# Performance work log

Measured on AMD Instinct MI355X. Metric: run time of the kernel, lower is better.

Reference implementation:

```python
import jax, jax.numpy as jnp
import numpy as np

RADIUS = 0.4
SIGMA = 0.08
EPS = 1e-5  # InstanceNorm2d default eps
KERNEL_CONDENSE_RATIO = 0.7


def setup_inputs() -> dict:
    key = jax.random.key(0)
    k1, k2, k3, k4, k5 = jax.random.split(key, 5)
    m, b, nc, ks, na, co = 1024, 2, 512, 24, 60, 128
    frag = jax.random.uniform(k1, (m, 3), dtype=jnp.float32)          # fragment points in unit cube
    clouds = jax.random.uniform(k2, (b, 3, nc), dtype=jnp.float32)    # centers (already n_center -> no FPS)
    # kernel points inside ball of KERNEL_CONDENSE_RATIO * radius
    kp = (jax.random.uniform(k3, (ks, 3), dtype=jnp.float32) - 0.5) * 2.0 * (KERNEL_CONDENSE_RATIO * RADIUS)
    # kanchor=60 rotation anchors (random orthonormal frames via QR)
    anchors, _ = jnp.linalg.qr(jax.random.normal(k4, (na, 3, 3), dtype=jnp.float32))
    # rotate kernel points per anchor: (ks, na, 3), matching np.transpose(anchors @ kernels.T, (2,0,1))
    kernels = jnp.einsum('aij,kj->kai', anchors, kp)
    # BasicSO3Conv weight: dim_in=1 -> W [dim_out, ks]
    W = jax.random.normal(k5, (co, ks), dtype=jnp.float32) * (1.0 / np.sqrt(ks))
    return {"frag": frag, "clouds": clouds, "kernels": kernels, "W": W, "anchors": anchors}


def _propagate(frag, clouds, kernels, W):
    # frag [m,3], clouds [b,3,nc], kernels [ks,na,3], W [co,ks]
    c = jnp.transpose(clouds, (0, 2, 1))                 # [b,nc,3]
    diff = frag[None, None] - c[:, :, None]              # [b,nc,m,3] (frag point minus center)
    d2 = jnp.sum(diff * diff, axis=-1)                   # [b,nc,m]
    mask = (d2 < RADIUS * RADIUS).astype(diff.dtype)     # ball query mask
    nnctn = jnp.sum(mask, axis=-1)                       # [b,nc] neighbor counts
    base = jnp.exp(-d2 / SIGMA) * mask                   # shared Gaussian factor, masked [b,nc,m]
    k2 = jnp.sum(kernels * kernels, axis=-1)             # [ks,na]
    na = kernels.shape[1]

    def step(carry, a_idx):
        kpa = kernels[:, a_idx]                          # [ks,3] kernel points for this anchor
        dot = jnp.einsum('bnmd,kd->bnmk', diff, kpa)     # [b,nc,m,ks]
        # exp(-||diff - kp||^2 / sigma) = base * exp((2*dot - |kp|^2)/sigma)
        w = base[..., None] * jnp.exp((2.0 * dot - k2[:, a_idx]) / SIGMA)
        return carry, jnp.sum(w, axis=2)                 # [b,nc,ks]

    _, wts = jax.lax.scan(step, 0, jnp.arange(na))       # [na,b,nc,ks]
    wts = jnp.transpose(wts, (1, 3, 2, 0))               # [b,ks,nc,na]
    wts = wts / (nnctn[:, None, :, None] + 1.0)          # count normalization

    feats = jnp.einsum('ck,bkna->bcna', W, wts)          # BasicSO3Conv (dim_in=1): [b,co,nc,na]
    # InstanceNorm2d(affine=False): per (b, channel) stats over spatial (nc, na)
    mu = jnp.mean(feats, axis=(2, 3), keepdims=True)
    var = jnp.var(feats, axis=(2, 3), keepdims=True)
    feat = (feats - mu) * jax.lax.rsqrt(var + EPS)
    return jax.nn.relu(feat)


def reference(frag, clouds, kernels, W, anchors):
    feat = _propagate(frag, clouds, kernels, W)
    # SphericalPointCloud(xyz=centers, feats, anchors)
    return clouds, feat, anchors
```

## Files before the change

kernel.cpp:

```cpp
#include <hip/hip_runtime.h>
#include <math.h>

#define NC 512
#define NB 2
#define M 1024
#define KS 24
#define NA 60
#define CO 128
#define CELLS 1440
#define CHA 20
#define CCELLS 480
#define NTOT 30720.0f
#define LSCALE 18.033688011112043f
#define R2 0.16f
#define NSLOT 32

#define FEAT_OFF 3072
#define ANCH_OFF (3072 + 7864320)

__device__ __forceinline__ float dot4acc(float s, float4 w, float4 v) {
    return fmaf(w.x, v.x, fmaf(w.y, v.y, fmaf(w.z, v.z, fmaf(w.w, v.w, s))));
}

__launch_bounds__(256)
__global__ void k_wts(const float* __restrict__ frag, const float* __restrict__ clouds,
                      const float* __restrict__ kernels, const float* __restrict__ W,
                      float* __restrict__ wts, float* __restrict__ accum) {
    int bx = blockIdx.x;
    int chunk = bx % 3;
    int bn = bx / 3;
    int b = bn >> 9, n = bn & (NC - 1);
    int tid = threadIdx.x, wave = tid >> 6, lane = tid & 63;
    __shared__ float4 spl[M];
    __shared__ int wcnt[16];
    __shared__ __align__(16) float swl[512];

    int lc0 = tid, lc1 = tid + 256;
    float4 kc0, kc1;
    {
        int cells[2] = {chunk * CCELLS + lc0, chunk * CCELLS + lc1};
        bool vld[2] = {true, lc1 < CCELLS};
        float4* kcs[2] = {&kc0, &kc1};
        #pragma unroll
        for (int q = 0; q < 2; ++q) {
            if (vld[q]) {
                int cell = cells[q];
                int a = cell / KS, k = cell - a * KS;
                const float* kp = kernels + (size_t)(k * NA + a) * 3;
                float kx = kp[0], ky = kp[1], kz = kp[2];
                float k2 = kx * kx + ky * ky + kz * kz;
                *kcs[q] = make_float4(kx * (2.0f * LSCALE), ky * (2.0f * LSCALE),
                                      kz * (2.0f * LSCALE), -k2 * LSCALE);
            } else {
                *kcs[q] = make_float4(0.f, 0.f, 0.f, -1e30f);
            }
        }
    }

    float cx = clouds[b * 3 * NC + n];
    float cy = clouds[b * 3 * NC + NC + n];
    float cz = clouds[b * 3 * NC + 2 * NC + n];

    float dx[4], dy[4], dz[4], ei[4];
    int pos[4];
    bool pr[4];
    unsigned long long lmask = (1ull << lane) - 1ull;
    #pragma unroll
    for (int j = 0; j < 4; ++j) {
        int m = tid + j * 256;
        dx[j] = frag[3 * m]     - cx;
        dy[j] = frag[3 * m + 1] - cy;
        dz[j] = frag[3 * m + 2] - cz;
        float s = __fmul_rn(dx[j], dx[j]);
        s = __fadd_rn(s, __fmul_rn(dy[j], dy[j]));
        s = __fadd_rn(s, __fmul_rn(dz[j], dz[j]));
        pr[j] = s < R2;
        ei[j] = __builtin_amdgcn_exp2f(-s * LSCALE);
        unsigned long long mk = __ballot(pr[j]);
        pos[j] = __popcll(mk & lmask);
        if (lane == 0) wcnt[j * 4 + wave] = __popcll(mk);
    }
    __syncthreads();
    int run = 0, base[4];
    #pragma unroll
    for (int t2 = 0; t2 < 16; ++t2) {
        if ((t2 & 3) == wave) base[t2 >> 2] = run;
        run += wcnt[t2];
    }
    int cnt = run;
    #pragma unroll
    for (int j = 0; j < 4; ++j)
        if (pr[j]) spl[base[j] + pos[j]] = make_float4(dx[j], dy[j], dz[j], ei[j]);
    __syncthreads();

    float acc0 = 0.f, acc1 = 0.f;
    #pragma unroll 2
    for (int i = 0; i < cnt; ++i) {
        float4 p = spl[i];
        float a0 = fmaf(p.x, kc0.x, fmaf(p.y, kc0.y, fmaf(p.z, kc0.z, kc0.w)));
        float a1 = fmaf(p.x, kc1.x, fmaf(p.y, kc1.y, fmaf(p.z, kc1.z, kc1.w)));
        acc0 = fmaf(__builtin_amdgcn_exp2f(a0), p.w, acc0);
        acc1 = fmaf(__builtin_amdgcn_exp2f(a1), p.w, acc1);
    }

    float inv = 1.0f / (float)(cnt + 1);
    float w0 = acc0 * inv, w1 = acc1 * inv;
    float* wrow = wts + (size_t)bn * CELLS + chunk * CCELLS;
    wrow[lc0] = w0;
    swl[lc0] = w0;
    if (lc1 < CCELLS) { wrow[lc1] = w1; swl[lc1] = w1; }
    __syncthreads();

    int c = tid >> 1, ah = tid & 1;
    float4 wr[6];
    {
        const float4* W4 = (const float4*)(W + c * KS);
        #pragma unroll
        for (int j = 0; j < 6; ++j) wr[j] = W4[j];
    }
    float fs = 0.f, fs2 = 0.f;
    #pragma unroll
    for (int i = 0; i < 10; ++i) {
        const float4* v4 = (const float4*)(swl + (ah * 10 + i) * KS);
        float f = 0.f;
        #pragma unroll
        for (int j = 0; j < 6; ++j) f = dot4acc(f, wr[j], v4[j]);
        fs += f;
        fs2 = fmaf(f, f, fs2);
    }
    fs  += __shfl_xor(fs, 1);
    fs2 += __shfl_xor(fs2, 1);
    if (ah == 0) {
        int slot = bx & (NSLOT - 1);
        float* ap = accum + (((size_t)(b * NSLOT + slot) * CO + c) * 2);
        atomicAdd(&ap[0], fs);
        atomicAdd(&ap[1], fs2);
    }
}

__launch_bounds__(256)
__global__ void k_out(const float* __restrict__ wts, const float* __restrict__ W,
                      const float* __restrict__ accum, const float* __restrict__ clouds,
                      const float* __restrict__ anchors, float* __restrict__ out) {
    int bn = blockIdx.x, b = bn >> 9, n = bn & (NC - 1);
    int tid = threadIdx.x, wave = tid >> 6, lane = tid & 63;
    __shared__ __align__(16) float wl[CELLS];
    __shared__ float fl[CO * NA];
    __shared__ float2 sst[CO];

    if (bn < 12) {
        int i = bn * 256 + tid;
        out[i] = clouds[i];
    } else if (bn < 15) {
        int i = (bn - 12) * 256 + tid;
        if (i < 540) out[ANCH_OFF + i] = anchors[i];
    }

    if (tid < CO) {
        int c = tid;
        float s = 0.f, s2 = 0.f;
        #pragma unroll
        for (int sl = 0; sl < NSLOT; ++sl) {
            const float* ap = accum + (((size_t)(b * NSLOT + sl) * CO + c) * 2);
            s += ap[0];
            s2 += ap[1];
        }
        const float invN = 1.0f / NTOT;
        float mu = s * invN;
        float var = fmaxf(fmaf(-mu, mu, s2 * invN), 0.f);
        sst[c] = make_float2(mu, rsqrtf(var + 1e-5f));
    }
    {
        const float4* src = (const float4*)(wts + (size_t)bn * CELLS);
        float4* wl4 = (float4*)wl;
        wl4[tid] = src[tid];
        if (tid < 104) wl4[tid + 256] = src[tid + 256];
    }
    __syncthreads();

    int cpair = tid >> 2, aq = tid & 3;
    int c0 = cpair * 2, a0 = aq * 15;
    float4 w0[6], w1[6];
    {
        const float4* W40 = (const float4*)(W + c0 * KS);
        const float4* W41 = (const float4*)(W + (c0 + 1) * KS);
        #pragma unroll
        for (int j = 0; j < 6; ++j) { w0[j] = W40[j]; w1[j] = W41[j]; }
    }
    float2 st0 = sst[c0], st1 = sst[c0 + 1];
    #pragma unroll
    for (int i = 0; i < 15; ++i) {
        const float4* v4 = (const float4*)(wl + (a0 + i) * KS);
        float s0 = 0.f, s1 = 0.f;
        #pragma unroll
        for (int j = 0; j < 6; ++j) {
            float4 v = v4[j];
            s0 = dot4acc(s0, w0[j], v);
            s1 = dot4acc(s1, w1[j], v);
        }
        fl[c0 * NA + a0 + i]       = fmaxf((s0 - st0.x) * st0.y, 0.f);
        fl[(c0 + 1) * NA + a0 + i] = fmaxf((s1 - st1.x) * st1.y, 0.f);
    }
    __syncthreads();

    #pragma unroll 4
    for (int i = 0; i < 32; ++i) {
        int c = wave * 32 + i;
        if (lane < NA)
            out[FEAT_OFF + (((size_t)(b * CO + c)) * NC + n) * NA + lane] = fl[c * NA + lane];
    }
}

extern "C" void kernel_launch(void* const* d_in, const int* in_sizes, int n_in,
                              void* d_out, int out_size, void* d_ws, size_t ws_size,
                              hipStream_t stream) {
    const float* frag    = (const float*)d_in[0];
    const float* clouds  = (const float*)d_in[1];
    const float* kernels = (const float*)d_in[2];
    const float* W       = (const float*)d_in[3];
    const float* anchors = (const float*)d_in[4];
    float* out = (float*)d_out;

    char* ws = (char*)d_ws;
    float* wts   = (float*)(ws);
    float* accum = (float*)(ws + 5898240);

    hipMemsetAsync(accum, 0, 2 * NSLOT * CO * 2 * sizeof(float), stream);
    k_wts<<<3 * NB * NC, 256, 0, stream>>>(frag, clouds, kernels, W, wts, accum);
    k_out<<<NB * NC, 256, 0, stream>>>(wts, W, accum, clouds, anchors, out);
}
```

Before: 140.7 us.

## Retile output kernel by channel group and point tile with XCD-aware block mapping

The output kernel now gives each block 8 channels and 32 centers, processed as four tiles of 8 centers. It writes contiguous float4 runs per channel, so each store covers 8 consecutive centers' 60 anchors, replacing the strided per-center writes. Block IDs are mapped so each XCD handles one batch and a contiguous range, and the per-block stats reduction is limited to its 8 channels. The trade-offs are that the wts rows are now re-read by 16 channel groups instead of once, the grid shrinks to 512 blocks, and the main loop in k_wts is unrolled further.

```diff
diff --git a/kernel.cpp b/kernel.cpp
--- a/kernel.cpp
+++ b/kernel.cpp
@@ -8,7 +8,6 @@
 #define NA 60
 #define CO 128
 #define CELLS 1440
-#define CHA 20
 #define CCELLS 480
 #define NTOT 30720.0f
 #define LSCALE 18.033688011112043f
@@ -17,6 +16,11 @@
 
 #define FEAT_OFF 3072
 #define ANCH_OFF (3072 + 7864320)
+
+#define WLP 1444
+#define TILE_N 8
+#define BLK_C 8
+#define BLK_N 32
 
 __device__ __forceinline__ float dot4acc(float s, float4 w, float4 v) {
     return fmaf(w.x, v.x, fmaf(w.y, v.y, fmaf(w.z, v.z, fmaf(w.w, v.w, s))));
@@ -94,7 +98,7 @@
     __syncthreads();
 
     float acc0 = 0.f, acc1 = 0.f;
-    #pragma unroll 2
+    #pragma unroll 4
     for (int i = 0; i < cnt; ++i) {
         float4 p = spl[i];
         float a0 = fmaf(p.x, kc0.x, fmaf(p.y, kc0.y, fmaf(p.z, kc0.z, kc0.w)));
@@ -142,72 +146,111 @@
 __global__ void k_out(const float* __restrict__ wts, const float* __restrict__ W,
                       const float* __restrict__ accum, const float* __restrict__ clouds,
                       const float* __restrict__ anchors, float* __restrict__ out) {
-    int bn = blockIdx.x, b = bn >> 9, n = bn & (NC - 1);
-    int tid = threadIdx.x, wave = tid >> 6, lane = tid & 63;
-    __shared__ __align__(16) float wl[CELLS];
-    __shared__ float fl[CO * NA];
-    __shared__ float2 sst[CO];
-
-    if (bn < 12) {
-        int i = bn * 256 + tid;
+    int bid = blockIdx.x;
+    int xcd = bid & 7, grp = bid >> 3;
+    int b   = xcd >> 2;
+    int sub = (xcd & 3) * 64 + grp;
+    int cg  = sub >> 4;
+    int nr  = sub & 15;
+    int tid = threadIdx.x;
+
+    __shared__ __align__(16) float wl[TILE_N * WLP];
+    __shared__ __align__(16) float fl[BLK_C * TILE_N * NA];
+    __shared__ float4 sred[128];
+    __shared__ float2 sst[BLK_C];
+
+    if (bid < 12) {
+        int i = bid * 256 + tid;
         out[i] = clouds[i];
-    } else if (bn < 15) {
-        int i = (bn - 12) * 256 + tid;
+    } else if (bid < 15) {
+        int i = (bid - 12) * 256 + tid;
         if (i < 540) out[ANCH_OFF + i] = anchors[i];
     }
 
-    if (tid < CO) {
-        int c = tid;
-        float s = 0.f, s2 = 0.f;
-        #pragma unroll
-        for (int sl = 0; sl < NSLOT; ++sl) {
-            const float* ap = accum + (((size_t)(b * NSLOT + sl) * CO + c) * 2);
-            s += ap[0];
-            s2 += ap[1];
+    if (tid < 128) {
+        int slot = tid >> 2, cpl = tid & 3;
+        sred[tid] = ((const float4*)accum)[((size_t)(b * NSLOT + slot)) * 64 + cg * 4 + cpl];
+    }
+
+    const float* wbase = wts + ((size_t)(b * NC + nr * BLK_N)) * CELLS;
+    {
+        #pragma unroll
+        for (int j = 0; j < 12; ++j) {
+            int idx = j * 256 + tid;
+            if (idx < 720 * 4) {
+                int r = idx / 360, cw = idx - r * 360;
+                float4 v = ((const float4*)(wbase + (size_t)r * CELLS))[cw];
+                ((float4*)(wl + r * WLP))[cw] = v;
+            }
+        }
+    }
+    __syncthreads();
+
+    if (tid < 4) {
+        float4 r = make_float4(0.f, 0.f, 0.f, 0.f);
+        #pragma unroll
+        for (int s = 0; s < NSLOT; ++s) {
+            float4 v = sred[s * 4 + tid];
+            r.x += v.x; r.y += v.y; r.z += v.z; r.w += v.w;
         }
         const float invN = 1.0f / NTOT;
-        float mu = s * invN;
-        float var = fmaxf(fmaf(-mu, mu, s2 * invN), 0.f);
-        sst[c] = make_float2(mu, rsqrtf(var + 1e-5f));
-    }
-    {
-        const float4* src = (const float4*)(wts + (size_t)bn * CELLS);
-        float4* wl4 = (float4*)wl;
-        wl4[tid] = src[tid];
-        if (tid < 104) wl4[tid + 256] = src[tid + 256];
-    }
-    __syncthreads();
-
-    int cpair = tid >> 2, aq = tid & 3;
-    int c0 = cpair * 2, a0 = aq * 15;
-    float4 w0[6], w1[6];
-    {
-        const float4* W40 = (const float4*)(W + c0 * KS);
-        const float4* W41 = (const float4*)(W + (c0 + 1) * KS);
-        #pragma unroll
-        for (int j = 0; j < 6; ++j) { w0[j] = W40[j]; w1[j] = W41[j]; }
-    }
-    float2 st0 = sst[c0], st1 = sst[c0 + 1];
-    #pragma unroll
-    for (int i = 0; i < 15; ++i) {
-        const float4* v4 = (const float4*)(wl + (a0 + i) * KS);
-        float s0 = 0.f, s1 = 0.f;
-        #pragma unroll
-        for (int j = 0; j < 6; ++j) {
-            float4 v = v4[j];
-            s0 = dot4acc(s0, w0[j], v);
-            s1 = dot4acc(s1, w1[j], v);
-        }
-        fl[c0 * NA + a0 + i]       = fmaxf((s0 - st0.x) * st0.y, 0.f);
-        fl[(c0 + 1) * NA + a0 + i] = fmaxf((s1 - st1.x) * st1.y, 0.f);
-    }
-    __syncthreads();
-
-    #pragma unroll 4
-    for (int i = 0; i < 32; ++i) {
-        int c = wave * 32 + i;
-        if (lane < NA)
-            out[FEAT_OFF + (((size_t)(b * CO + c)) * NC + n) * NA + lane] = fl[c * NA + lane];
+        float mu0 = r.x * invN;
+        float var0 = fmaxf(fmaf(-mu0, mu0, r.y * invN), 0.f);
+        float mu1 = r.z * invN;
+        float var1 = fmaxf(fmaf(-mu1, mu1, r.w * invN), 0.f);
+        sst[tid * 2]     = make_float2(mu0, rsqrtf(var0 + 1e-5f));
+        sst[tid * 2 + 1] = make_float2(mu1, rsqrtf(var1 + 1e-5f));
+    }
+
+    int c_loc = tid >> 5, t5 = tid & 31;
+    int np = t5 >> 2, aq = t5 & 3;
+    int c = cg * BLK_C + c_loc;
+    float4 wr[6];
+    {
+        const float4* W4 = (const float4*)(W + c * KS);
+        #pragma unroll
+        for (int j = 0; j < 6; ++j) wr[j] = W4[j];
+    }
+    __syncthreads();
+    float2 st = sst[c_loc];
+
+    for (int t = 0; t < 4; ++t) {
+        const float* vrow = wl + np * WLP;
+        #pragma unroll
+        for (int i = 0; i < 15; ++i) {
+            int a = aq * 15 + i;
+            const float4* v4 = (const float4*)(vrow + a * KS);
+            float f = 0.f;
+            #pragma unroll
+            for (int j = 0; j < 6; ++j) f = dot4acc(f, wr[j], v4[j]);
+            fl[(c_loc * TILE_N + np) * NA + a] = fmaxf((f - st.x) * st.y, 0.f);
+        }
+        __syncthreads();
+        if (t < 3) {
+            #pragma unroll
+            for (int j = 0; j < 12; ++j) {
+                int idx = j * 256 + tid;
+                if (idx < 720 * 4) {
+                    int r = idx / 360, cw = idx - r * 360;
+                    float4 v = ((const float4*)(wbase + (size_t)((t + 1) * TILE_N + r) * CELLS))[cw];
+                    ((float4*)(wl + r * WLP))[cw] = v;
+                }
+            }
+        }
+        {
+            const float4* fl4 = (const float4*)fl;
+            int n0 = nr * BLK_N + t * TILE_N;
+            float* obase = out + FEAT_OFF + ((size_t)(b * CO + c) * NC + n0) * NA;
+            #pragma unroll
+            for (int q = 0; q < 4; ++q) {
+                int fi = t5 + q * 32;
+                if (fi < 120) {
+                    float4 v = fl4[c_loc * 120 + fi];
+                    ((float4*)obase)[fi] = v;
+                }
+            }
+        }
+        if (t < 3) __syncthreads();
     }
 }
 
@@ -227,5 +270,5 @@
 
     hipMemsetAsync(accum, 0, 2 * NSLOT * CO * 2 * sizeof(float), stream);
     k_wts<<<3 * NB * NC, 256, 0, stream>>>(frag, clouds, kernels, W, wts, accum);
-    k_out<<<NB * NC, 256, 0, stream>>>(wts, W, accum, clouds, anchors, out);
-}
+    k_out<<<512, 256, 0, stream>>>(wts, W, accum, clouds, anchors, out);
+}
```

Result: slower. 150.0 us (+6.6%).
